# Kernel tuning notes

Measured on AMD Instinct MI355X. Metric: run time of the kernel, lower is better.

Reference implementation:

```python
import jax, jax.numpy as jnp
import numpy as np
from jax import lax

D_MODEL = 192
D_STATE = 128
D_CONV = 3
EXPAND = 2
HEADDIM = 64
NGROUPS = 1
CHUNK = 256
K = 4  # scan directions
D_INNER = EXPAND * D_MODEL          # 384
D_SSM = D_INNER                     # 384
NHEADS = D_SSM // HEADDIM           # 6
HH = K * NHEADS                     # 24 heads total (dir-major)
CONV_CH = D_SSM + 2 * NGROUPS * D_STATE + NHEADS  # 646 (conv applied to x,B,C,dt channels)
D_IN_PROJ = 2 * D_INNER + 2 * NGROUPS * D_STATE + NHEADS  # 1030
BSZ, HIMG, WIMG = 4, 64, 64


def setup_inputs() -> dict:
    key = jax.random.key(0)
    ks = jax.random.split(key, 8)
    u = jax.random.normal(ks[0], (BSZ, HIMG, WIMG, D_MODEL), jnp.float32)
    W_in = jax.random.normal(ks[1], (D_MODEL, D_IN_PROJ), jnp.float32) * 0.02
    conv_w = jax.random.normal(ks[2], (CONV_CH, 1, D_CONV, D_CONV), jnp.float32) * 0.1
    conv_b = jnp.zeros((CONV_CH,), jnp.float32)
    # dt_bias init per source: inverse-softplus of dt ~ LogUniform(1e-3, 1e-1), tiled over 4 dirs
    dt = jnp.exp(jax.random.uniform(ks[3], (NHEADS,)) * (np.log(0.1) - np.log(0.001)) + np.log(0.001))
    dt = jnp.maximum(dt, 1e-4)
    inv_dt = dt + jnp.log(-jnp.expm1(-dt))
    dt_bias = jnp.tile(inv_dt[None, :], (K, 1))  # (4, nheads)
    A = jax.random.uniform(ks[4], (NHEADS,), minval=1.0, maxval=16.0)
    A_logs = jnp.tile(jnp.log(A), (K,))          # (24,)
    Ds = jnp.ones((HH,), jnp.float32)
    norm_w = jnp.ones((D_SSM,), jnp.float32)
    W_out = jax.random.normal(ks[5], (D_INNER, D_MODEL), jnp.float32) * 0.02
    return dict(u=u, W_in=W_in, conv_w=conv_w, conv_b=conv_b, dt_bias=dt_bias,
                A_logs=A_logs, Ds=Ds, norm_w=norm_w, W_out=W_out)


def _ssd(x, dt, A, Bm, Cm, chunk):
    """Chunked selective state-space scan (Mamba2 SSD).
    x: (b,L,H,P), dt: (b,L,H) (post-softplus), A: (H,) negative scalars,
    Bm/Cm: (b,L,G,N) with heads grouped G-major (H = G*hpg)."""
    b, L, H, P = x.shape
    G, N = Bm.shape[2], Bm.shape[3]
    hpg = H // G
    nc = L // chunk
    x = x.reshape(b, nc, chunk, G, hpg, P)
    dt = dt.reshape(b, nc, chunk, G, hpg)
    Bm = Bm.reshape(b, nc, chunk, G, N)
    Cm = Cm.reshape(b, nc, chunk, G, N)
    dA = dt * A.reshape(G, hpg)                 # (b,z,c,g,h), negative
    dAc = jnp.cumsum(dA, axis=2)                # within-chunk cumsum
    dAt = jnp.transpose(dAc, (0, 1, 3, 4, 2))   # (b,z,g,h,c)
    idx = jnp.arange(chunk)
    mask = idx[:, None] >= idx[None, :]         # causal within chunk
    seg = jnp.exp(jnp.where(mask, dAt[..., :, None] - dAt[..., None, :], -1e30))  # (b,z,g,h,c,s)
    CB = jnp.einsum('bzcgn,bzsgn->bzgcs', Cm, Bm)
    xdt = x * dt[..., None]                     # dt applied at source position
    y_intra = jnp.einsum('bzghcs,bzsghp->bzcghp', CB[:, :, :, None] * seg, xdt)
    decay_last = jnp.exp(dAc[:, :, -1:] - dAc)  # (b,z,c,g,h)
    states = jnp.einsum('bzcgn,bzcghp->bzghpn', Bm, xdt * decay_last[..., None])
    cd = jnp.exp(dAc[:, :, -1])                 # (b,z,g,h) whole-chunk decay

    def step(carry, inp):
        s, c = inp
        return carry * c[..., None, None] + s, carry  # emit state entering the chunk

    _, prevs = lax.scan(step, jnp.zeros_like(states[:, 0]),
                        (jnp.swapaxes(states, 0, 1), jnp.swapaxes(cd, 0, 1)))
    prev = jnp.swapaxes(prevs, 0, 1)            # (b,z,g,h,P,N)
    y_inter = jnp.einsum('bzcgn,bzghpn->bzcghp', Cm, prev) * jnp.exp(dAc)[..., None]
    return (y_intra + y_inter).reshape(b, L, H, P)


def reference(u, W_in, conv_w, conv_b, dt_bias, A_logs, Ds, norm_w, W_out):
    B, H, W, C = u.shape
    L = H * W
    zxbcdt = u @ W_in                            # (B,H,W,1030); d_mlp == 0
    z = zxbcdt[..., :D_SSM]                      # gate
    xBCdt = zxbcdt[..., D_SSM:]                  # (B,H,W,CONV_CH)
    # depthwise 3x3 conv + SiLU (NCHW)
    xb = jnp.transpose(xBCdt, (0, 3, 1, 2))
    xb = lax.conv_general_dilated(xb, conv_w, (1, 1), 'SAME',
                                  feature_group_count=CONV_CH,
                                  dimension_numbers=('NCHW', 'OIHW', 'NCHW'))
    xb = jax.nn.silu(xb + conv_b[None, :, None, None])
    # 4 scan directions: row-major, col-major, and their reverses
    d0 = xb.reshape(B, CONV_CH, L)
    d1 = jnp.transpose(xb, (0, 1, 3, 2)).reshape(B, CONV_CH, L)
    dirs = jnp.stack([d0, d1], axis=1)
    dirs = jnp.concatenate([dirs, jnp.flip(dirs, axis=-1)], axis=1)  # (B,4,CONV_CH,L)
    seq = jnp.transpose(dirs, (0, 3, 1, 2))      # (B,L,4,CONV_CH)
    xs = seq[..., :D_SSM].reshape(B, L, HH, HEADDIM)
    Bs = seq[..., D_SSM:D_SSM + D_STATE]         # (B,L,4,N), ngroups=1 -> G=4 dirs
    Cs = seq[..., D_SSM + D_STATE:D_SSM + 2 * D_STATE]
    dts = seq[..., D_SSM + 2 * D_STATE:].reshape(B, L, HH)
    dt = jax.nn.softplus(dts + dt_bias.reshape(HH))
    A = -jnp.exp(A_logs)                         # (HH,)
    y = _ssd(xs, dt, A, Bs, Cs, CHUNK) + xs * Ds[None, None, :, None]
    y = y.reshape(B, L, K, D_SSM)
    y0 = y[:, :, 0]
    y1 = y[:, :, 1]
    y2 = jnp.flip(y[:, :, 2], axis=1)
    y3 = jnp.flip(y[:, :, 3], axis=1)
    wh1 = jnp.transpose(y1.reshape(B, W, H, D_SSM), (0, 2, 1, 3)).reshape(B, L, D_SSM)
    wh3 = jnp.transpose(y3.reshape(B, W, H, D_SSM), (0, 2, 1, 3)).reshape(B, L, D_SSM)
    out = (y0 + y2 + wh1 + wh3).reshape(B, H, W, D_SSM)
    # RMSNormGated (norm_before_gate=False, group_size = d_ssm)
    g = out * jax.nn.silu(z)
    g = g * lax.rsqrt(jnp.mean(g * g, axis=-1, keepdims=True) + 1e-5) * norm_w
    return g @ W_out
```

## Files before the change

kernel.cpp:

```cpp
#include <hip/hip_runtime.h>
#include <hip/hip_fp16.h>
#include <math.h>

#define BQ 4
#define LQ 4096
#define DM 192
#define DIP 1030
#define DSSM 384
#define DST 128
#define CCH 646
#define CH640 640
#define NHD 6
#define KDIR 4
#define NCH 16
#define CLEN 256
#define UH_ELEMS (16384 * 192)
#define WT_ELEMS (1152 * 192)

using half8 = __attribute__((ext_vector_type(8))) _Float16;
using half4 = __attribute__((ext_vector_type(4))) _Float16;
using f32x4 = __attribute__((ext_vector_type(4))) float;

#define XWI(pp, ss) ((pp) * 72 + ((((ss) >> 3) ^ ((pp) >> 3)) << 3) + ((ss) & 7))
#define XW2(n, ss) ((n) * 72 + (((((ss) >> 3) ^ ((n) >> 3)) & 7) << 3) + ((ss) & 7))

__device__ __forceinline__ int pixof(int k, int t) {
  switch (k) {
    case 0: return t;
    case 1: return ((t & 63) << 6) | (t >> 6);
    case 2: return 4095 - t;
    default: { int tp = 4095 - t; return ((tp & 63) << 6) | (tp >> 6); }
  }
}

__device__ __forceinline__ float softplusf(float x) {
  return (x > 20.f) ? x : log1pf(expf(x));
}
__device__ __forceinline__ float siluf(float x) {
  return x / (1.f + __expf(-x));
}

__global__ void k_cvt(const float* __restrict__ u, const float* __restrict__ W,
                      _Float16* __restrict__ uh, _Float16* __restrict__ whT) {
  int idx = blockIdx.x * 256 + threadIdx.x;
  if (idx < UH_ELEMS) uh[idx] = (_Float16)u[idx];
  int widx = idx - UH_ELEMS;
  if (widx >= 0 && widx < WT_ELEMS) {
    int n = widx / 192, kk = widx - n * 192;
    whT[widx] = (n < DIP) ? (_Float16)W[(size_t)kk * DIP + n] : (_Float16)0.f;
  }
}

__global__ __launch_bounds__(256) void k_inproj(
    const _Float16* __restrict__ uh, const _Float16* __restrict__ whT,
    __half* __restrict__ zh, __half* __restrict__ xbch, float* __restrict__ xdt32) {
  __shared__ __align__(16) _Float16 sA[128 * 72];
  __shared__ __align__(16) _Float16 sB[128 * 72];
  int nt = blockIdx.x, mt = blockIdx.y;
  int m0 = mt * 128, n0 = nt * 128;
  int t = threadIdx.x, lane = t & 63, w = t >> 6;
  int acol = lane & 15, koff = (lane >> 4) * 8;
  int wr = w >> 1, wc = w & 1;
  f32x4 zz = {0.f, 0.f, 0.f, 0.f};
  f32x4 acc[4][4];
#pragma unroll
  for (int fr = 0; fr < 4; ++fr)
#pragma unroll
    for (int fc = 0; fc < 4; ++fc) acc[fr][fc] = zz;
  for (int kk = 0; kk < 3; ++kk) {
    if (kk) __syncthreads();
#pragma unroll
    for (int i = 0; i < 4; ++i) {
      int task = t + i * 256;
      int row = task >> 3, oct = task & 7;
      *(half8*)&sA[row * 72 + oct * 8] =
          *(const half8*)&uh[(size_t)(m0 + row) * 192 + kk * 64 + oct * 8];
      *(half8*)&sB[row * 72 + oct * 8] =
          *(const half8*)&whT[(size_t)(n0 + row) * 192 + kk * 64 + oct * 8];
    }
    __syncthreads();
#pragma unroll
    for (int ks = 0; ks < 2; ++ks) {
      half8 af[4], bf[4];
#pragma unroll
      for (int f = 0; f < 4; ++f) {
        af[f] = *(const half8*)&sA[(wr * 64 + f * 16 + acol) * 72 + ks * 32 + koff];
        bf[f] = *(const half8*)&sB[(wc * 64 + f * 16 + acol) * 72 + ks * 32 + koff];
      }
#pragma unroll
      for (int fr = 0; fr < 4; ++fr)
#pragma unroll
        for (int fc = 0; fc < 4; ++fc)
          acc[fr][fc] = __builtin_amdgcn_mfma_f32_16x16x32_f16(af[fr], bf[fc], acc[fr][fc], 0, 0, 0);
    }
  }
  int rb = (lane >> 4) * 4;
#pragma unroll
  for (int fr = 0; fr < 4; ++fr) {
#pragma unroll
    for (int fc = 0; fc < 4; ++fc) {
      int n = n0 + wc * 64 + fc * 16 + acol;
#pragma unroll
      for (int r = 0; r < 4; ++r) {
        int m = m0 + wr * 64 + fr * 16 + rb + r;
        float v = acc[fr][fc][r];
        if (n < DSSM) zh[(size_t)m * DSSM + n] = (__half)v;
        else if (n < 1024) xbch[(size_t)m * CH640 + (n - DSSM)] = (__half)v;
        else if (n < DIP) xdt32[(size_t)m * NHD + (n - 1024)] = v;
      }
    }
  }
}

__global__ void k_conv(const __half* __restrict__ xbch, const float* __restrict__ xdt,
                       const float* __restrict__ cw, const float* __restrict__ cb,
                       __half* __restrict__ convh, float* __restrict__ dtraw) {
  int pid = blockIdx.x;
  int b = pid >> 12, p = pid & 4095;
  int y = p >> 6, x = p & 63;
  int t = threadIdx.x;
  const __half2* baseh2 = (const __half2*)(xbch + (size_t)b * LQ * CH640);
  __half2* outh2 = (__half2*)(convh + (size_t)pid * CH640);
  for (int pc = t; pc < 320; pc += 256) {
    int c0 = pc * 2;
    float s0 = 0.f, s1 = 0.f;
#pragma unroll
    for (int ky = 0; ky < 3; ++ky) {
      int yy = y + ky - 1;
      if (yy < 0 || yy > 63) continue;
#pragma unroll
      for (int kx = 0; kx < 3; ++kx) {
        int xx = x + kx - 1;
        if (xx < 0 || xx > 63) continue;
        __half2 v = baseh2[(size_t)(yy * 64 + xx) * 320 + pc];
        int wi = ky * 3 + kx;
        s0 += (float)v.x * cw[c0 * 9 + wi];
        s1 += (float)v.y * cw[(c0 + 1) * 9 + wi];
      }
    }
    __half2 o;
    o.x = (__half)siluf(s0 + cb[c0]);
    o.y = (__half)siluf(s1 + cb[c0 + 1]);
    outh2[pc] = o;
  }
  if (t < NHD) {
    const float* based = xdt + (size_t)b * LQ * NHD;
    float s = 0.f;
#pragma unroll
    for (int ky = 0; ky < 3; ++ky) {
      int yy = y + ky - 1;
      if (yy < 0 || yy > 63) continue;
#pragma unroll
      for (int kx = 0; kx < 3; ++kx) {
        int xx = x + kx - 1;
        if (xx < 0 || xx > 63) continue;
        s += based[(size_t)(yy * 64 + xx) * NHD + t] * cw[(CH640 + t) * 9 + ky * 3 + kx];
      }
    }
    dtraw[(size_t)pid * NHD + t] = siluf(s + cb[CH640 + t]);
  }
}

__global__ void k_prep(const float* __restrict__ dtraw, const float* __restrict__ dt_bias,
                       const float* __restrict__ A_logs,
                       float* __restrict__ dtb, float* __restrict__ dacb) {
  __shared__ float sb[CLEN];
  int z = blockIdx.x, k = blockIdx.y, b = blockIdx.z;
  int s = threadIdx.x;
  int pixel = pixof(k, z * CLEN + s);
  const float* row = dtraw + ((size_t)(b * LQ + pixel)) * NHD;
  float raw[NHD];
#pragma unroll
  for (int h = 0; h < NHD; ++h) raw[h] = row[h];
  size_t base = (((size_t)(b * KDIR + k) * NCH + z) * NHD) * CLEN;
  for (int h = 0; h < NHD; ++h) {
    float dtv = softplusf(raw[h] + dt_bias[k * NHD + h]);
    float dA = dtv * (-expf(A_logs[k * NHD + h]));
    sb[s] = dA;
    __syncthreads();
    for (int off = 1; off < CLEN; off <<= 1) {
      float v = (s >= off) ? sb[s - off] : 0.f;
      __syncthreads();
      sb[s] += v;
      __syncthreads();
    }
    dtb[base + (size_t)h * CLEN + s] = dtv;
    dacb[base + (size_t)h * CLEN + s] = sb[s];
    __syncthreads();
  }
}

__global__ __launch_bounds__(256, 4) void k_cb(const _Float16* __restrict__ convh,
                                               _Float16* __restrict__ cbuf) {
  __shared__ __align__(16) char smem[34816];
  _Float16* sCt = (_Float16*)smem;
  _Float16* sBt = (_Float16*)(smem + 17408);
  int pi = blockIdx.x, z = blockIdx.y, bk = blockIdx.z;
  int b = bk >> 2, kd = bk & 3;
  int SI = 0;
  while ((SI + 1) * (SI + 2) / 2 <= pi) ++SI;
  int SJ = pi - SI * (SI + 1) / 2;
  int t = threadIdx.x, lane = t & 63, w = t >> 6;
  int acol = lane & 15, koff = (lane >> 4) * 8;
  int R = w * 16, arow = R + acol, rbase = R + (lane >> 4) * 4;
  const _Float16* convb = convh + (size_t)b * LQ * CH640;
  for (int i = 0; i < 4; ++i) {
    int c = t + i * 256;
    int row = c >> 4, seg = c & 15;
    int pc = pixof(kd, z * CLEN + SI * 64 + row);
    *(half8*)&sCt[row * 136 + seg * 8] =
        *(const half8*)&convb[(size_t)pc * CH640 + (DSSM + DST) + seg * 8];
    int pbx = pixof(kd, z * CLEN + SJ * 64 + row);
    *(half8*)&sBt[row * 136 + seg * 8] =
        *(const half8*)&convb[(size_t)pbx * CH640 + DSSM + seg * 8];
  }
  __syncthreads();
  f32x4 zz = {0.f, 0.f, 0.f, 0.f};
  f32x4 acc[4] = {zz, zz, zz, zz};
  for (int ks = 0; ks < 4; ++ks) {
    half8 a = *(const half8*)&sCt[arow * 136 + ks * 32 + koff];
#pragma unroll
    for (int cg = 0; cg < 4; ++cg) {
      half8 bf = *(const half8*)&sBt[(cg * 16 + acol) * 136 + ks * 32 + koff];
      acc[cg] = __builtin_amdgcn_mfma_f32_16x16x32_f16(a, bf, acc[cg], 0, 0, 0);
    }
  }
  size_t base = ((size_t)(bk * NCH + z) * 10 + pi) * 4096;
#pragma unroll
  for (int cg = 0; cg < 4; ++cg)
#pragma unroll
    for (int r = 0; r < 4; ++r)
      cbuf[base + (size_t)(rbase + r) * 64 + cg * 16 + acol] = (_Float16)acc[cg][r];
}

__global__ __launch_bounds__(256, 4) void k_states(
    const _Float16* __restrict__ convh, const float* __restrict__ dtb,
    const float* __restrict__ dacb, float* __restrict__ statesT) {
  __shared__ __align__(16) _Float16 sA[64 * 72];
  __shared__ __align__(16) _Float16 sB2[128 * 72];
  __shared__ float sFac[CLEN];
  int h = blockIdx.x, z = blockIdx.y, bk = blockIdx.z;
  int b = bk >> 2, kd = bk & 3;
  int t = threadIdx.x, lane = t & 63, w = t >> 6;
  int acol = lane & 15, koct = lane >> 4;
  size_t dbase = (((size_t)bk * NCH + z) * NHD + h) * CLEN;
  {
    float dac_last = dacb[dbase + CLEN - 1];
    sFac[t] = dtb[dbase + t] * __expf(dac_last - dacb[dbase + t]);
  }
  __syncthreads();
  const _Float16* convb = convh + (size_t)b * LQ * CH640;
  f32x4 zz = {0.f, 0.f, 0.f, 0.f};
  f32x4 acc[8] = {zz, zz, zz, zz, zz, zz, zz, zz};
  for (int st = 0; st < 4; ++st) {
    if (st) __syncthreads();
#pragma unroll
    for (int i = 0; i < 2; ++i) {
      int c = t + i * 256;
      int ss = c >> 3, pp0 = (c & 7) * 8;
      int sg = st * 64 + ss;
      int px = pixof(kd, z * CLEN + sg);
      half8 xv = *(const half8*)&convb[(size_t)px * CH640 + h * 64 + pp0];
      float f = sFac[sg];
#pragma unroll
      for (int u = 0; u < 8; ++u) sA[XWI(pp0 + u, ss)] = (_Float16)((float)xv[u] * f);
    }
#pragma unroll
    for (int i = 0; i < 4; ++i) {
      int c = t + i * 256;
      int ss = c >> 4, n0 = (c & 15) * 8;
      int sg = st * 64 + ss;
      int px = pixof(kd, z * CLEN + sg);
      half8 bv = *(const half8*)&convb[(size_t)px * CH640 + DSSM + n0];
#pragma unroll
      for (int u = 0; u < 8; ++u) sB2[XW2(n0 + u, ss)] = bv[u];
    }
    __syncthreads();
#pragma unroll
    for (int ks = 0; ks < 2; ++ks) {
      int kso = ks * 4 + koct;
      int arow = w * 16 + acol;
      half8 a = *(const half8*)&sA[arow * 72 + ((kso ^ (arow >> 3)) << 3)];
#pragma unroll
      for (int nf = 0; nf < 8; ++nf) {
        int col = nf * 16 + acol;
        half8 bf = *(const half8*)&sB2[col * 72 + (((kso ^ (col >> 3)) & 7) << 3)];
        acc[nf] = __builtin_amdgcn_mfma_f32_16x16x32_f16(a, bf, acc[nf], 0, 0, 0);
      }
    }
  }
  size_t sbase = (((size_t)bk * NCH + z) * NHD + h) * (128 * 64);
  int rbase = koct * 4;
#pragma unroll
  for (int nf = 0; nf < 8; ++nf) {
    int col = nf * 16 + acol;
#pragma unroll
    for (int r = 0; r < 4; ++r)
      statesT[sbase + (size_t)(w * 16 + rbase + r) * 128 + col] = acc[nf][r];
  }
}

__global__ void k_scan(float* __restrict__ states, const float* __restrict__ dacb) {
  int h = blockIdx.x, k = blockIdx.y, b = blockIdx.z;
  int bk = b * KDIR + k;
  int t = threadIdx.x;
  float carry[32];
#pragma unroll
  for (int j = 0; j < 32; ++j) carry[j] = 0.f;
  for (int z = 0; z < NCH; ++z) {
    float cd = __expf(dacb[(((size_t)bk * NCH + z) * NHD + h) * CLEN + (CLEN - 1)]);
    size_t sbase = (((size_t)bk * NCH + z) * NHD + h) * (128 * 64);
#pragma unroll
    for (int j = 0; j < 32; ++j) {
      size_t idx = sbase + (size_t)j * 256 + t;
      float sv = states[idx];
      states[idx] = carry[j];
      carry[j] = carry[j] * cd + sv;
    }
  }
}

__global__ __launch_bounds__(256, 4) void k_y(
    const _Float16* __restrict__ convh, const float* __restrict__ dtb,
    const float* __restrict__ dacb, const _Float16* __restrict__ cbuf,
    const float* __restrict__ prevT, const float* __restrict__ Ds,
    _Float16* __restrict__ ybuf) {
  __shared__ __align__(16) char smem[34816];
  __shared__ float sdt[CLEN], sdac[CLEN], sFac[CLEN];
  __shared__ float sExpD[64], sRs[64];
  _Float16* sC = (_Float16*)smem;
  _Float16* sPrev = (_Float16*)(smem + 17408);
  _Float16* sA = (_Float16*)smem;
  _Float16* sXW = (_Float16*)(smem + 9216);

  int wg = blockIdx.x;
  int xid = (wg & 7) * 768 + (wg >> 3);
  int grp = xid / 24, i24 = xid % 24;
  int h = i24 >> 2, si_t = i24 & 3;
  int bk = grp >> 4, z = grp & 15;
  int b = bk >> 2, kd = bk & 3;
  int t = threadIdx.x;
  int lane = t & 63, w = t >> 6;
  int acol = lane & 15, koff = (lane >> 4) * 8;
  int R = w * 16, arow = R + acol, rbase = R + (lane >> 4) * 4;

  size_t dbase = (((size_t)bk * NCH + z) * NHD + h) * CLEN;
  sdt[t] = dtb[dbase + t];
  sdac[t] = dacb[dbase + t];
  __syncthreads();
  float ref = sdac[si_t * 64];
  sFac[t] = __expf(ref - sdac[t]);
  if (t < 64) {
    float d = sdac[si_t * 64 + t];
    sExpD[t] = __expf(d);
    sRs[t] = __expf(d - ref);
  }
  const _Float16* convb = convh + (size_t)b * LQ * CH640;
  for (int i = 0; i < 4; ++i) {
    int c = t + i * 256;
    int row = c >> 4, seg = c & 15;
    int px = pixof(kd, z * CLEN + si_t * 64 + row);
    *(half8*)&sC[row * 136 + seg * 8] =
        *(const half8*)&convb[(size_t)px * CH640 + (DSSM + DST) + seg * 8];
  }
  const float* pbp = prevT + (((size_t)bk * NCH + z) * NHD + h) * (128 * 64);
  for (int i = 0; i < 8; ++i) {
    int idx = t + i * 256;
    int p = idx >> 5, n0 = (idx & 31) * 4;
    float4 v = *(const float4*)&pbp[(size_t)p * 128 + n0];
    half4 hv;
    hv[0] = (_Float16)v.x; hv[1] = (_Float16)v.y;
    hv[2] = (_Float16)v.z; hv[3] = (_Float16)v.w;
    *(half4*)&sPrev[p * 136 + n0] = hv;
  }
  __syncthreads();
  f32x4 zz = {0.f, 0.f, 0.f, 0.f};
  f32x4 accE[4] = {zz, zz, zz, zz};
  for (int ks = 0; ks < 4; ++ks) {
    half8 a = *(const half8*)&sC[arow * 136 + ks * 32 + koff];
#pragma unroll
    for (int cg = 0; cg < 4; ++cg) {
      half8 bf = *(const half8*)&sPrev[(cg * 16 + acol) * 136 + ks * 32 + koff];
      accE[cg] = __builtin_amdgcn_mfma_f32_16x16x32_f16(a, bf, accE[cg], 0, 0, 0);
    }
  }
  __syncthreads();
  f32x4 accI[4] = {zz, zz, zz, zz};
  for (int SJ = 0; SJ < si_t; ++SJ) {
    for (int i = 0; i < 2; ++i) {
      int c = t + i * 256;
      int ss = c >> 3, pp0 = (c & 7) * 8;
      int sg = SJ * 64 + ss;
      int px = pixof(kd, z * CLEN + sg);
      half8 xv = *(const half8*)&convb[(size_t)px * CH640 + h * 64 + pp0];
      float f = sdt[sg] * sFac[sg];
#pragma unroll
      for (int u = 0; u < 8; ++u)
        sXW[XWI(pp0 + u, ss)] = (_Float16)((float)xv[u] * f);
    }
    __syncthreads();
    size_t cbase = ((size_t)(bk * NCH + z) * 10 + si_t * (si_t + 1) / 2 + SJ) * 4096;
#pragma unroll
    for (int ks = 0; ks < 2; ++ks) {
      half8 a = *(const half8*)&cbuf[cbase + (size_t)arow * 64 + ks * 32 + koff];
      int kso = ks * 4 + (lane >> 4);
#pragma unroll
      for (int cg = 0; cg < 4; ++cg) {
        int col = cg * 16 + acol;
        half8 bf = *(const half8*)&sXW[col * 72 + ((kso ^ (col >> 3)) << 3)];
        accI[cg] = __builtin_amdgcn_mfma_f32_16x16x32_f16(a, bf, accI[cg], 0, 0, 0);
      }
    }
    __syncthreads();
  }
  {
    float rsv[4];
#pragma unroll
    for (int r = 0; r < 4; ++r) rsv[r] = sRs[rbase + r];
#pragma unroll
    for (int cg = 0; cg < 4; ++cg)
#pragma unroll
      for (int r = 0; r < 4; ++r) accI[cg][r] *= rsv[r];
  }
  {
    size_t cbase = ((size_t)(bk * NCH + z) * 10 + si_t * (si_t + 1) / 2 + si_t) * 4096;
    for (int i = 0; i < 16; ++i) {
      int e = t + i * 256;
      int sl = e >> 6, ss = e & 63;
      float cv = 0.f;
      if (ss <= sl)
        cv = (float)cbuf[cbase + e] * __expf(sdac[si_t * 64 + sl] - sdac[si_t * 64 + ss]);
      sA[sl * 72 + ss] = (_Float16)cv;
    }
    for (int i = 0; i < 2; ++i) {
      int c = t + i * 256;
      int ss = c >> 3, pp0 = (c & 7) * 8;
      int sg = si_t * 64 + ss;
      int px = pixof(kd, z * CLEN + sg);
      half8 xv = *(const half8*)&convb[(size_t)px * CH640 + h * 64 + pp0];
      float f = sdt[sg];
#pragma unroll
      for (int u = 0; u < 8; ++u)
        sXW[XWI(pp0 + u, ss)] = (_Float16)((float)xv[u] * f);
    }
    __syncthreads();
#pragma unroll
    for (int ks = 0; ks < 2; ++ks) {
      half8 a = *(const half8*)&sA[arow * 72 + ks * 32 + koff];
      int kso = ks * 4 + (lane >> 4);
#pragma unroll
      for (int cg = 0; cg < 4; ++cg) {
        int col = cg * 16 + acol;
        half8 bf = *(const half8*)&sXW[col * 72 + ((kso ^ (col >> 3)) << 3)];
        accI[cg] = __builtin_amdgcn_mfma_f32_16x16x32_f16(a, bf, accI[cg], 0, 0, 0);
      }
    }
  }
  float dsv = Ds[kd * NHD + h];
  float eD[4];
#pragma unroll
  for (int r = 0; r < 4; ++r) eD[r] = sExpD[rbase + r];
#pragma unroll
  for (int cg = 0; cg < 4; ++cg) {
    int col = cg * 16 + acol;
#pragma unroll
    for (int r = 0; r < 4; ++r) {
      int row = rbase + r;
      int tg = z * CLEN + si_t * 64 + row;
      int px = pixof(kd, tg);
      float xv = (float)convb[(size_t)px * CH640 + h * 64 + col];
      float yv = accI[cg][r] + eD[r] * accE[cg][r] + dsv * xv;
      ybuf[((size_t)bk * LQ + tg) * DSSM + h * 64 + col] = (_Float16)yv;
    }
  }
}

__global__ void k_final(const __half* __restrict__ yb, const __half* __restrict__ zh,
                        const float* __restrict__ norm_w, const float* __restrict__ Wout,
                        float* __restrict__ out) {
  __shared__ float sg[8 * DSSM];
  __shared__ float srstd[8];
  int m0 = blockIdx.x * 8;
  int t = threadIdx.x;
  for (int rr = 0; rr < 8; ++rr) {
    int m = m0 + rr, b = m >> 12, px = m & 4095;
    int tr = ((px & 63) << 6) | (px >> 6);
    int t0 = px, t1 = tr, t2 = 4095 - px, t3 = 4095 - tr;
    size_t b4 = (size_t)b * 4;
    for (int c = t; c < DSSM; c += 256) {
      float yv = (float)yb[((b4 + 0) * LQ + t0) * DSSM + c] +
                 (float)yb[((b4 + 1) * LQ + t1) * DSSM + c] +
                 (float)yb[((b4 + 2) * LQ + t2) * DSSM + c] +
                 (float)yb[((b4 + 3) * LQ + t3) * DSSM + c];
      float zv = (float)zh[(size_t)m * DSSM + c];
      sg[rr * DSSM + c] = yv * (zv / (1.f + __expf(-zv)));
    }
  }
  __syncthreads();
  {
    int r = t >> 5, j = t & 31;
    float s = 0.f;
    for (int c = j; c < DSSM; c += 32) { float g = sg[r * DSSM + c]; s += g * g; }
    s += __shfl_xor(s, 16, 32);
    s += __shfl_xor(s, 8, 32);
    s += __shfl_xor(s, 4, 32);
    s += __shfl_xor(s, 2, 32);
    s += __shfl_xor(s, 1, 32);
    if (j == 0) srstd[r] = rsqrtf(s / (float)DSSM + 1e-5f);
  }
  __syncthreads();
  for (int rr = 0; rr < 8; ++rr)
    for (int c = t; c < DSSM; c += 256) sg[rr * DSSM + c] *= srstd[rr] * norm_w[c];
  __syncthreads();
  if (t < DM) {
    float a[8];
#pragma unroll
    for (int rr = 0; rr < 8; ++rr) a[rr] = 0.f;
    for (int c = 0; c < DSSM; ++c) {
      float wv = Wout[(size_t)c * DM + t];
#pragma unroll
      for (int rr = 0; rr < 8; ++rr) a[rr] += sg[rr * DSSM + c] * wv;
    }
#pragma unroll
    for (int rr = 0; rr < 8; ++rr) out[(size_t)(m0 + rr) * DM + t] = a[rr];
  }
}

extern "C" void kernel_launch(void* const* d_in, const int* in_sizes, int n_in,
                              void* d_out, int out_size, void* d_ws, size_t ws_size,
                              hipStream_t stream) {
  const float* u = (const float*)d_in[0];
  const float* W_in = (const float*)d_in[1];
  const float* conv_w = (const float*)d_in[2];
  const float* conv_b = (const float*)d_in[3];
  const float* dt_bias = (const float*)d_in[4];
  const float* A_logs = (const float*)d_in[5];
  const float* Ds = (const float*)d_in[6];
  const float* norm_w = (const float*)d_in[7];
  const float* W_out = (const float*)d_in[8];
  float* out = (float*)d_out;

  float* ws = (float*)d_ws;
  size_t off = 0;
  __half* zh = (__half*)(ws + off); off += (size_t)BQ * LQ * DSSM / 2;
  _Float16* uh = (_Float16*)(ws + off); off += (size_t)UH_ELEMS / 2;
  _Float16* whT = (_Float16*)(ws + off); off += (size_t)WT_ELEMS / 2;
  __half* xbch = (__half*)(ws + off); off += (size_t)BQ * LQ * CH640 / 2;
  float* xdt32 = ws + off; off += (size_t)BQ * LQ * NHD;
  __half* convh = (__half*)(ws + off); off += (size_t)BQ * LQ * CH640 / 2;
  float* dtraw = ws + off; off += (size_t)BQ * LQ * NHD;
  float* dtb = ws + off; off += (size_t)BQ * KDIR * NCH * NHD * CLEN;
  float* dacb = ws + off; off += (size_t)BQ * KDIR * NCH * NHD * CLEN;
  float* statesT = ws + off; off += (size_t)BQ * KDIR * NCH * NHD * 128 * 64;
  __half* ybuf = (__half*)(ws + off); off += (size_t)BQ * KDIR * LQ * DSSM / 2;
  _Float16* cbuf = (_Float16*)xbch;

  k_cvt<<<(UH_ELEMS + WT_ELEMS) / 256, 256, 0, stream>>>(u, W_in, uh, whT);
  k_inproj<<<dim3(9, 128), 256, 0, stream>>>(uh, whT, zh, xbch, xdt32);
  k_conv<<<BQ * LQ, 256, 0, stream>>>(xbch, xdt32, conv_w, conv_b, convh, dtraw);
  k_prep<<<dim3(NCH, KDIR, BQ), 256, 0, stream>>>(dtraw, dt_bias, A_logs, dtb, dacb);
  k_cb<<<dim3(10, NCH, BQ * KDIR), 256, 0, stream>>>((const _Float16*)convh, cbuf);
  k_states<<<dim3(NHD, NCH, BQ * KDIR), 256, 0, stream>>>((const _Float16*)convh, dtb, dacb, statesT);
  k_scan<<<dim3(NHD, KDIR, BQ), 256, 0, stream>>>(statesT, dacb);
  k_y<<<KDIR * NHD * 4 * NCH * BQ, 256, 0, stream>>>((const _Float16*)convh, dtb, dacb,
                                                     (const _Float16*)cbuf, statesT, Ds,
                                                     (_Float16*)ybuf);
  k_final<<<BQ * LQ / 8, 256, 0, stream>>>(ybuf, zh, norm_w, W_out, out);
}
```

Baseline: 480.0 us.

## Store chunk states in fp16 and loop all sub-tiles per k_y block

Chunk states are now written and carried through the inter-chunk scan in fp16 instead of fp32, which halves that buffer's traffic in k_states, k_scan and k_y. k_y now launches one block per (batch, direction, chunk, head) and loops over the four 64-row sub-tiles inside the block, so the previous-state tile is loaded into LDS once rather than four times. The C operand for the inter-chunk term is read straight from global memory instead of being staged in LDS. In exchange, grid parallelism drops by a factor of four and each block runs longer and less evenly. Rounding the scan carry to fp16 at every chunk adds precision risk.

```diff
diff --git a/kernel.cpp b/kernel.cpp
--- a/kernel.cpp
+++ b/kernel.cpp
@@ -235,7 +235,7 @@
 
 __global__ __launch_bounds__(256, 4) void k_states(
     const _Float16* __restrict__ convh, const float* __restrict__ dtb,
-    const float* __restrict__ dacb, float* __restrict__ statesT) {
+    const float* __restrict__ dacb, _Float16* __restrict__ statesT) {
   __shared__ __align__(16) _Float16 sA[64 * 72];
   __shared__ __align__(16) _Float16 sB2[128 * 72];
   __shared__ float sFac[CLEN];
@@ -296,11 +296,11 @@
     int col = nf * 16 + acol;
 #pragma unroll
     for (int r = 0; r < 4; ++r)
-      statesT[sbase + (size_t)(w * 16 + rbase + r) * 128 + col] = acc[nf][r];
-  }
-}
-
-__global__ void k_scan(float* __restrict__ states, const float* __restrict__ dacb) {
+      statesT[sbase + (size_t)(w * 16 + rbase + r) * 128 + col] = (_Float16)acc[nf][r];
+  }
+}
+
+__global__ void k_scan(_Float16* __restrict__ states, const float* __restrict__ dacb) {
   int h = blockIdx.x, k = blockIdx.y, b = blockIdx.z;
   int bk = b * KDIR + k;
   int t = threadIdx.x;
@@ -313,8 +313,8 @@
 #pragma unroll
     for (int j = 0; j < 32; ++j) {
       size_t idx = sbase + (size_t)j * 256 + t;
-      float sv = states[idx];
-      states[idx] = carry[j];
+      float sv = (float)states[idx];
+      states[idx] = (_Float16)carry[j];
       carry[j] = carry[j] * cd + sv;
     }
   }
@@ -323,154 +323,143 @@
 __global__ __launch_bounds__(256, 4) void k_y(
     const _Float16* __restrict__ convh, const float* __restrict__ dtb,
     const float* __restrict__ dacb, const _Float16* __restrict__ cbuf,
-    const float* __restrict__ prevT, const float* __restrict__ Ds,
+    const _Float16* __restrict__ prevT, const float* __restrict__ Ds,
     _Float16* __restrict__ ybuf) {
-  __shared__ __align__(16) char smem[34816];
+  __shared__ __align__(16) _Float16 sPrev[64 * 136];
+  __shared__ __align__(16) _Float16 sXW[64 * 72];
+  __shared__ __align__(16) _Float16 sA[64 * 72];
   __shared__ float sdt[CLEN], sdac[CLEN], sFac[CLEN];
   __shared__ float sExpD[64], sRs[64];
-  _Float16* sC = (_Float16*)smem;
-  _Float16* sPrev = (_Float16*)(smem + 17408);
-  _Float16* sA = (_Float16*)smem;
-  _Float16* sXW = (_Float16*)(smem + 9216);
 
   int wg = blockIdx.x;
-  int xid = (wg & 7) * 768 + (wg >> 3);
-  int grp = xid / 24, i24 = xid % 24;
-  int h = i24 >> 2, si_t = i24 & 3;
-  int bk = grp >> 4, z = grp & 15;
+  int xid = (wg & 7) * 192 + (wg >> 3);
+  int h = xid % 6;
+  int bkz = xid / 6;
+  int bk = bkz >> 4, z = bkz & 15;
   int b = bk >> 2, kd = bk & 3;
-  int t = threadIdx.x;
-  int lane = t & 63, w = t >> 6;
+  int t = threadIdx.x, lane = t & 63, w = t >> 6;
   int acol = lane & 15, koff = (lane >> 4) * 8;
   int R = w * 16, arow = R + acol, rbase = R + (lane >> 4) * 4;
 
   size_t dbase = (((size_t)bk * NCH + z) * NHD + h) * CLEN;
   sdt[t] = dtb[dbase + t];
   sdac[t] = dacb[dbase + t];
+  const _Float16* pbp = prevT + (((size_t)bk * NCH + z) * NHD + h) * (128 * 64);
+#pragma unroll
+  for (int i = 0; i < 4; ++i) {
+    int idx = t + i * 256;
+    int p = idx >> 4, seg = idx & 15;
+    *(half8*)&sPrev[p * 136 + seg * 8] = *(const half8*)&pbp[(size_t)p * 128 + seg * 8];
+  }
   __syncthreads();
-  float ref = sdac[si_t * 64];
-  sFac[t] = __expf(ref - sdac[t]);
-  if (t < 64) {
-    float d = sdac[si_t * 64 + t];
-    sExpD[t] = __expf(d);
-    sRs[t] = __expf(d - ref);
-  }
   const _Float16* convb = convh + (size_t)b * LQ * CH640;
-  for (int i = 0; i < 4; ++i) {
-    int c = t + i * 256;
-    int row = c >> 4, seg = c & 15;
-    int px = pixof(kd, z * CLEN + si_t * 64 + row);
-    *(half8*)&sC[row * 136 + seg * 8] =
-        *(const half8*)&convb[(size_t)px * CH640 + (DSSM + DST) + seg * 8];
-  }
-  const float* pbp = prevT + (((size_t)bk * NCH + z) * NHD + h) * (128 * 64);
-  for (int i = 0; i < 8; ++i) {
-    int idx = t + i * 256;
-    int p = idx >> 5, n0 = (idx & 31) * 4;
-    float4 v = *(const float4*)&pbp[(size_t)p * 128 + n0];
-    half4 hv;
-    hv[0] = (_Float16)v.x; hv[1] = (_Float16)v.y;
-    hv[2] = (_Float16)v.z; hv[3] = (_Float16)v.w;
-    *(half4*)&sPrev[p * 136 + n0] = hv;
-  }
-  __syncthreads();
+  float dsv = Ds[kd * NHD + h];
   f32x4 zz = {0.f, 0.f, 0.f, 0.f};
-  f32x4 accE[4] = {zz, zz, zz, zz};
-  for (int ks = 0; ks < 4; ++ks) {
-    half8 a = *(const half8*)&sC[arow * 136 + ks * 32 + koff];
+
+  for (int si_t = 0; si_t < 4; ++si_t) {
+    float ref = sdac[si_t * 64];
+    sFac[t] = __expf(ref - sdac[t]);
+    if (t < 64) {
+      float d = sdac[si_t * 64 + t];
+      sExpD[t] = __expf(d);
+      sRs[t] = __expf(d - ref);
+    }
+    __syncthreads();
+    float eD[4], rsv[4];
+#pragma unroll
+    for (int r = 0; r < 4; ++r) { eD[r] = sExpD[rbase + r]; rsv[r] = sRs[rbase + r]; }
+    f32x4 accE[4] = {zz, zz, zz, zz};
+    f32x4 accI[4] = {zz, zz, zz, zz};
+    int pxa = pixof(kd, z * CLEN + si_t * 64 + arow);
+#pragma unroll
+    for (int ks = 0; ks < 4; ++ks) {
+      half8 a = *(const half8*)&convb[(size_t)pxa * CH640 + (DSSM + DST) + ks * 32 + koff];
+#pragma unroll
+      for (int cg = 0; cg < 4; ++cg) {
+        half8 bf = *(const half8*)&sPrev[(cg * 16 + acol) * 136 + ks * 32 + koff];
+        accE[cg] = __builtin_amdgcn_mfma_f32_16x16x32_f16(a, bf, accE[cg], 0, 0, 0);
+      }
+    }
+    for (int SJ = 0; SJ < si_t; ++SJ) {
+#pragma unroll
+      for (int i = 0; i < 2; ++i) {
+        int c = t + i * 256;
+        int ss = c >> 3, pp0 = (c & 7) * 8;
+        int sg = SJ * 64 + ss;
+        int px = pixof(kd, z * CLEN + sg);
+        half8 xv = *(const half8*)&convb[(size_t)px * CH640 + h * 64 + pp0];
+        float f = sdt[sg] * sFac[sg];
+#pragma unroll
+        for (int u = 0; u < 8; ++u)
+          sXW[XWI(pp0 + u, ss)] = (_Float16)((float)xv[u] * f);
+      }
+      __syncthreads();
+      size_t cbase = ((size_t)(bk * NCH + z) * 10 + si_t * (si_t + 1) / 2 + SJ) * 4096;
+#pragma unroll
+      for (int ks = 0; ks < 2; ++ks) {
+        half8 a = *(const half8*)&cbuf[cbase + (size_t)arow * 64 + ks * 32 + koff];
+        int kso = ks * 4 + (lane >> 4);
+#pragma unroll
+        for (int cg = 0; cg < 4; ++cg) {
+          int col = cg * 16 + acol;
+          half8 bf = *(const half8*)&sXW[col * 72 + ((kso ^ (col >> 3)) << 3)];
+          accI[cg] = __builtin_amdgcn_mfma_f32_16x16x32_f16(a, bf, accI[cg], 0, 0, 0);
+        }
+      }
+      __syncthreads();
+    }
+#pragma unroll
+    for (int cg = 0; cg < 4; ++cg)
+#pragma unroll
+      for (int r = 0; r < 4; ++r) accI[cg][r] *= rsv[r];
+    {
+      size_t cbase = ((size_t)(bk * NCH + z) * 10 + si_t * (si_t + 1) / 2 + si_t) * 4096;
+#pragma unroll
+      for (int i = 0; i < 16; ++i) {
+        int e = t + i * 256;
+        int sl = e >> 6, ss = e & 63;
+        float cv = 0.f;
+        if (ss <= sl)
+          cv = (float)cbuf[cbase + e] * __expf(sdac[si_t * 64 + sl] - sdac[si_t * 64 + ss]);
+        sA[sl * 72 + ss] = (_Float16)cv;
+      }
+#pragma unroll
+      for (int i = 0; i < 2; ++i) {
+        int c = t + i * 256;
+        int ss = c >> 3, pp0 = (c & 7) * 8;
+        int sg = si_t * 64 + ss;
+        int px = pixof(kd, z * CLEN + sg);
+        half8 xv = *(const half8*)&convb[(size_t)px * CH640 + h * 64 + pp0];
+        float f = sdt[sg];
+#pragma unroll
+        for (int u = 0; u < 8; ++u)
+          sXW[XWI(pp0 + u, ss)] = (_Float16)((float)xv[u] * f);
+      }
+      __syncthreads();
+#pragma unroll
+      for (int ks = 0; ks < 2; ++ks) {
+        half8 a = *(const half8*)&sA[arow * 72 + ks * 32 + koff];
+        int kso = ks * 4 + (lane >> 4);
+#pragma unroll
+        for (int cg = 0; cg < 4; ++cg) {
+          int col = cg * 16 + acol;
+          half8 bf = *(const half8*)&sXW[col * 72 + ((kso ^ (col >> 3)) << 3)];
+          accI[cg] = __builtin_amdgcn_mfma_f32_16x16x32_f16(a, bf, accI[cg], 0, 0, 0);
+        }
+      }
+    }
 #pragma unroll
     for (int cg = 0; cg < 4; ++cg) {
-      half8 bf = *(const half8*)&sPrev[(cg * 16 + acol) * 136 + ks * 32 + koff];
-      accE[cg] = __builtin_amdgcn_mfma_f32_16x16x32_f16(a, bf, accE[cg], 0, 0, 0);
-    }
-  }
-  __syncthreads();
-  f32x4 accI[4] = {zz, zz, zz, zz};
-  for (int SJ = 0; SJ < si_t; ++SJ) {
-    for (int i = 0; i < 2; ++i) {
-      int c = t + i * 256;
-      int ss = c >> 3, pp0 = (c & 7) * 8;
-      int sg = SJ * 64 + ss;
-      int px = pixof(kd, z * CLEN + sg);
-      half8 xv = *(const half8*)&convb[(size_t)px * CH640 + h * 64 + pp0];
-      float f = sdt[sg] * sFac[sg];
-#pragma unroll
-      for (int u = 0; u < 8; ++u)
-        sXW[XWI(pp0 + u, ss)] = (_Float16)((float)xv[u] * f);
-    }
-    __syncthreads();
-    size_t cbase = ((size_t)(bk * NCH + z) * 10 + si_t * (si_t + 1) / 2 + SJ) * 4096;
-#pragma unroll
-    for (int ks = 0; ks < 2; ++ks) {
-      half8 a = *(const half8*)&cbuf[cbase + (size_t)arow * 64 + ks * 32 + koff];
-      int kso = ks * 4 + (lane >> 4);
-#pragma unroll
-      for (int cg = 0; cg < 4; ++cg) {
-        int col = cg * 16 + acol;
-        half8 bf = *(const half8*)&sXW[col * 72 + ((kso ^ (col >> 3)) << 3)];
-        accI[cg] = __builtin_amdgcn_mfma_f32_16x16x32_f16(a, bf, accI[cg], 0, 0, 0);
-      }
-    }
-    __syncthreads();
-  }
-  {
-    float rsv[4];
-#pragma unroll
-    for (int r = 0; r < 4; ++r) rsv[r] = sRs[rbase + r];
-#pragma unroll
-    for (int cg = 0; cg < 4; ++cg)
-#pragma unroll
-      for (int r = 0; r < 4; ++r) accI[cg][r] *= rsv[r];
-  }
-  {
-    size_t cbase = ((size_t)(bk * NCH + z) * 10 + si_t * (si_t + 1) / 2 + si_t) * 4096;
-    for (int i = 0; i < 16; ++i) {
-      int e = t + i * 256;
-      int sl = e >> 6, ss = e & 63;
-      float cv = 0.f;
-      if (ss <= sl)
-        cv = (float)cbuf[cbase + e] * __expf(sdac[si_t * 64 + sl] - sdac[si_t * 64 + ss]);
-      sA[sl * 72 + ss] = (_Float16)cv;
-    }
-    for (int i = 0; i < 2; ++i) {
-      int c = t + i * 256;
-      int ss = c >> 3, pp0 = (c & 7) * 8;
-      int sg = si_t * 64 + ss;
-      int px = pixof(kd, z * CLEN + sg);
-      half8 xv = *(const half8*)&convb[(size_t)px * CH640 + h * 64 + pp0];
-      float f = sdt[sg];
-#pragma unroll
-      for (int u = 0; u < 8; ++u)
-        sXW[XWI(pp0 + u, ss)] = (_Float16)((float)xv[u] * f);
-    }
-    __syncthreads();
-#pragma unroll
-    for (int ks = 0; ks < 2; ++ks) {
-      half8 a = *(const half8*)&sA[arow * 72 + ks * 32 + koff];
-      int kso = ks * 4 + (lane >> 4);
-#pragma unroll
-      for (int cg = 0; cg < 4; ++cg) {
-        int col = cg * 16 + acol;
-        half8 bf = *(const half8*)&sXW[col * 72 + ((kso ^ (col >> 3)) << 3)];
-        accI[cg] = __builtin_amdgcn_mfma_f32_16x16x32_f16(a, bf, accI[cg], 0, 0, 0);
-      }
-    }
-  }
-  float dsv = Ds[kd * NHD + h];
-  float eD[4];
-#pragma unroll
-  for (int r = 0; r < 4; ++r) eD[r] = sExpD[rbase + r];
-#pragma unroll
-  for (int cg = 0; cg < 4; ++cg) {
-    int col = cg * 16 + acol;
-#pragma unroll
-    for (int r = 0; r < 4; ++r) {
-      int row = rbase + r;
-      int tg = z * CLEN + si_t * 64 + row;
-      int px = pixof(kd, tg);
-      float xv = (float)convb[(size_t)px * CH640 + h * 64 + col];
-      float yv = accI[cg][r] + eD[r] * accE[cg][r] + dsv * xv;
-      ybuf[((size_t)bk * LQ + tg) * DSSM + h * 64 + col] = (_Float16)yv;
+      int col = cg * 16 + acol;
+#pragma unroll
+      for (int r = 0; r < 4; ++r) {
+        int row = rbase + r;
+        int tg = z * CLEN + si_t * 64 + row;
+        int px = pixof(kd, tg);
+        float xv = (float)convb[(size_t)px * CH640 + h * 64 + col];
+        float yv = accI[cg][r] + eD[r] * accE[cg][r] + dsv * xv;
+        ybuf[((size_t)bk * LQ + tg) * DSSM + h * 64 + col] = (_Float16)yv;
+      }
     }
   }
 }
@@ -551,7 +540,7 @@
   float* dtraw = ws + off; off += (size_t)BQ * LQ * NHD;
   float* dtb = ws + off; off += (size_t)BQ * KDIR * NCH * NHD * CLEN;
   float* dacb = ws + off; off += (size_t)BQ * KDIR * NCH * NHD * CLEN;
-  float* statesT = ws + off; off += (size_t)BQ * KDIR * NCH * NHD * 128 * 64;
+  _Float16* statesT = (_Float16*)(ws + off); off += (size_t)BQ * KDIR * NCH * NHD * 128 * 64 / 2;
   __half* ybuf = (__half*)(ws + off); off += (size_t)BQ * KDIR * LQ * DSSM / 2;
   _Float16* cbuf = (_Float16*)xbch;
 
@@ -562,8 +551,8 @@
   k_cb<<<dim3(10, NCH, BQ * KDIR), 256, 0, stream>>>((const _Float16*)convh, cbuf);
   k_states<<<dim3(NHD, NCH, BQ * KDIR), 256, 0, stream>>>((const _Float16*)convh, dtb, dacb, statesT);
   k_scan<<<dim3(NHD, KDIR, BQ), 256, 0, stream>>>(statesT, dacb);
-  k_y<<<KDIR * NHD * 4 * NCH * BQ, 256, 0, stream>>>((const _Float16*)convh, dtb, dacb,
-                                                     (const _Float16*)cbuf, statesT, Ds,
-                                                     (_Float16*)ybuf);
+  k_y<<<BQ * KDIR * NCH * NHD, 256, 0, stream>>>((const _Float16*)convh, dtb, dacb,
+                                                 (const _Float16*)cbuf, statesT, Ds,
+                                                 (_Float16*)ybuf);
   k_final<<<BQ * LQ / 8, 256, 0, stream>>>(ybuf, zh, norm_w, W_out, out);
 }
```

After: 491.8 us. 2.5% more time.
